# Kernel tuning notes

Measured on AMD Instinct MI355X. Metric: run time of the kernel, lower is better.

Reference implementation:

```python
import jax, jax.numpy as jnp
import numpy as np

H = 2048      # hidden_size
NH = 16       # num_heads
HD = H // NH  # head_dim
B, T = 2, 2048


def setup_inputs() -> dict:
    key = jax.random.key(0)
    ks = jax.random.split(key, 5)
    s = 1.0 / np.sqrt(H)
    return {
        "x": jax.random.normal(ks[0], (B, T, H), dtype=jnp.float32),
        "wq": jax.random.normal(ks[1], (H, H), dtype=jnp.float32) * s,
        "bq": jnp.zeros((H,), dtype=jnp.float32),
        "wk": jax.random.normal(ks[2], (H, H), dtype=jnp.float32) * s,
        "bk": jnp.zeros((H,), dtype=jnp.float32),
        "wv": jax.random.normal(ks[3], (H, H), dtype=jnp.float32) * s,
        "bv": jnp.zeros((H,), dtype=jnp.float32),
        "wo": jax.random.normal(ks[4], (H, H), dtype=jnp.float32) * s,
        "bo": jnp.zeros((H,), dtype=jnp.float32),
    }


def reference(x, wq, bq, wk, bk, wv, bv, wo, bo):
    Bx, Tx, C = x.shape
    # projections (torch Linear: x @ W.T + b)
    q = x @ wq.T + bq
    k = x @ wk.T + bk
    v = x @ wv.T + bv
    # [B, T, H] -> [B, NH, T, HD]
    q = q.reshape(Bx, Tx, NH, HD).transpose(0, 2, 1, 3)
    k = k.reshape(Bx, Tx, NH, HD).transpose(0, 2, 1, 3)
    v = v.reshape(Bx, Tx, NH, HD).transpose(0, 2, 1, 3)
    scale = 1.0 / np.sqrt(HD).astype(np.float32)
    scores = jnp.einsum('bhqd,bhkd->bhqk', q, k) * scale  # [B, NH, T, T]
    causal = jnp.tril(jnp.ones((Tx, Tx), dtype=bool))
    scores = jnp.where(causal[None, None], scores, -jnp.inf)
    attn = jax.nn.softmax(scores, axis=-1)
    out = jnp.einsum('bhqk,bhkd->bhqd', attn, v)  # [B, NH, T, HD]
    out = out.transpose(0, 2, 1, 3).reshape(Bx, Tx, C)
    return out @ wo.T + bo
```

## Files before the change

kernel.cpp:

```cpp
#include <hip/hip_runtime.h>
#include <stdint.h>

constexpr int H_  = 2048;
constexpr int NH_ = 16;
constexpr int HD_ = 128;
constexpr int B_  = 2;
constexpr int T_  = 2048;
constexpr int M_  = B_ * T_;

typedef unsigned short u16;
typedef __bf16 bf16x8 __attribute__((ext_vector_type(8)));
typedef float  f32x4  __attribute__((ext_vector_type(4)));

constexpr float C1_ = 0.08838834764831845f * 1.4426950408889634f;

template <int N> struct IC { static constexpr int value = N; };

__device__ __forceinline__ u16 f2bf(float f) {
  uint32_t u = __builtin_bit_cast(uint32_t, f);
  u += 0x7fffu + ((u >> 16) & 1u);
  return (u16)(u >> 16);
}

__device__ __forceinline__ uint32_t cvtpk(float lo, float hi) {
  uint32_t r;
  asm("v_cvt_pk_bf16_f32 %0, %1, %2" : "=v"(r) : "v"(lo), "v"(hi));
  return r;
}

__device__ __forceinline__ void gload_lds16(const void* g, void* lds) {
  auto gp = (const __attribute__((address_space(1))) uint32_t*)(uintptr_t)g;
  auto lp = (__attribute__((address_space(3))) uint32_t*)(uint32_t)(uintptr_t)lds;
  __builtin_amdgcn_global_load_lds(gp, lp, 16, 0, 0);
}

__device__ __forceinline__ f32x4 mfma16(bf16x8 a, bf16x8 b, f32x4 c) {
  return __builtin_amdgcn_mfma_f32_16x16x32_bf16(a, b, c, 0, 0, 0);
}

__global__ __launch_bounds__(512) void cvt5_kernel(
    const float4* __restrict__ x,  const float4* __restrict__ wq,
    const float4* __restrict__ wk, const float4* __restrict__ wv,
    const float4* __restrict__ wo, ushort4* __restrict__ dst) {
  const int bid = blockIdx.x, tid = threadIdx.x;
  const float4* src;
  size_t idx, dof;
  if (bid < 4096) {
    src = x; idx = (size_t)bid * 512 + tid; dof = 0;
  } else {
    int w = (bid - 4096) >> 11;
    int r = (bid - 4096) & 2047;
    idx = (size_t)r * 512 + tid;
    dof = 2097152u + (size_t)w * 1048576u;
    src = (w == 0) ? wq : (w == 1) ? wk : (w == 2) ? wv : wo;
  }
  float4 v = src[idx];
  ushort4 o;
  o.x = f2bf(v.x); o.y = f2bf(v.y); o.z = f2bf(v.z); o.w = f2bf(v.w);
  dst[dof + idx] = o;
}

__device__ __forceinline__ void gemm256_core(const u16* __restrict__ A,
                                             const u16* __restrict__ Bm,
                                             const float* __restrict__ bias,
                                             void* __restrict__ Cout,
                                             int bid, int outmode,
                                             float oscale) {
  __shared__ u16 As[3][256 * 64];
  __shared__ u16 Bs[3][128 * 64];
  constexpr int Kg = H_;
  constexpr int NT = Kg / 64;
  const int tid = threadIdx.x;
  const int wave = tid >> 6, lane = tid & 63, l15 = lane & 15, lhi = lane >> 4;
  const int tm = bid & 15, tn = bid >> 4;
  const int m0 = tm << 8, n0 = tn << 7;
  const int wr = wave >> 1, wc = wave & 1;

  f32x4 acc[4][4] = {};

  const u16* pA[4];
  const u16* pB[2];
  {
    int o = tid * 16;
    int row = o >> 7;
    int sw  = o ^ ((row & 7) << 4);
    int c8  = (sw >> 4) & 7;
#pragma unroll
    for (int a = 0; a < 4; ++a)
      pA[a] = A + (size_t)(m0 + a * 64 + row) * Kg + c8 * 8;
#pragma unroll
    for (int a = 0; a < 2; ++a)
      pB[a] = Bm + (size_t)(n0 + a * 64 + row) * Kg + c8 * 8;
  }
  const int ldsoff = wave * 1024;

  int obA[2][4], obB[2][4];
#pragma unroll
  for (int kk = 0; kk < 2; ++kk) {
#pragma unroll
    for (int mi = 0; mi < 4; ++mi) {
      int rowA = wr * 64 + mi * 16 + l15;
      obA[kk][mi] = (rowA * 128 + kk * 64 + lhi * 16) ^ ((rowA & 7) << 4);
      int rowB = wc * 64 + mi * 16 + l15;
      obB[kk][mi] = (rowB * 128 + kk * 64 + lhi * 16) ^ ((rowB & 7) << 4);
    }
  }

  auto stageA = [&](int kt, auto bufc, int a) {
    constexpr int BUF = decltype(bufc)::value;
    gload_lds16(pA[a] + kt * 64,
                (char*)&As[BUF][0] + a * 8192 + ldsoff);
  };
  auto stageB = [&](int kt, auto bufc, int a) {
    constexpr int BUF = decltype(bufc)::value;
    gload_lds16(pB[a] + kt * 64,
                (char*)&Bs[BUF][0] + a * 8192 + ldsoff);
  };

  stageB(0, IC<0>{}, 0); stageB(0, IC<0>{}, 1);
  stageA(0, IC<0>{}, 0); stageA(0, IC<0>{}, 1);
  stageA(0, IC<0>{}, 2); stageA(0, IC<0>{}, 3);
  stageB(1, IC<1>{}, 0); stageB(1, IC<1>{}, 1);
  stageA(1, IC<1>{}, 0); stageA(1, IC<1>{}, 1);
  stageA(1, IC<1>{}, 2); stageA(1, IC<1>{}, 3);
  asm volatile("s_waitcnt vmcnt(6)" ::: "memory");
  __builtin_amdgcn_s_barrier();
  asm volatile("" ::: "memory");

  auto tile = [&](int kt, auto bufc) {
    constexpr int BUF = decltype(bufc)::value;
    constexpr int NXT = (BUF + 2) % 3;
    const bool hn2 = (kt + 2 < NT);
    const char* Ab = (const char*)&As[BUF][0];
    const char* Bb = (const char*)&Bs[BUF][0];
    bf16x8 a0, a1, b0, b1, b2, b3;

    a0 = *(const bf16x8*)(Ab + obA[0][0]); a1 = *(const bf16x8*)(Ab + obA[0][1]);
    b0 = *(const bf16x8*)(Bb + obB[0][0]); b1 = *(const bf16x8*)(Bb + obB[0][1]);
    b2 = *(const bf16x8*)(Bb + obB[0][2]); b3 = *(const bf16x8*)(Bb + obB[0][3]);
    if (hn2) { stageB(kt + 2, IC<NXT>{}, 0); stageB(kt + 2, IC<NXT>{}, 1); }
    __builtin_amdgcn_s_barrier(); asm volatile("" ::: "memory");
    __builtin_amdgcn_s_setprio(1);
    acc[0][0] = mfma16(a0, b0, acc[0][0]); acc[0][1] = mfma16(a0, b1, acc[0][1]);
    acc[0][2] = mfma16(a0, b2, acc[0][2]); acc[0][3] = mfma16(a0, b3, acc[0][3]);
    acc[1][0] = mfma16(a1, b0, acc[1][0]); acc[1][1] = mfma16(a1, b1, acc[1][1]);
    acc[1][2] = mfma16(a1, b2, acc[1][2]); acc[1][3] = mfma16(a1, b3, acc[1][3]);
    __builtin_amdgcn_s_setprio(0);
    __builtin_amdgcn_s_barrier(); asm volatile("" ::: "memory");

    a0 = *(const bf16x8*)(Ab + obA[0][2]); a1 = *(const bf16x8*)(Ab + obA[0][3]);
    if (hn2) { stageA(kt + 2, IC<NXT>{}, 0); stageA(kt + 2, IC<NXT>{}, 1); }
    __builtin_amdgcn_s_barrier(); asm volatile("" ::: "memory");
    __builtin_amdgcn_s_setprio(1);
    acc[2][0] = mfma16(a0, b0, acc[2][0]); acc[2][1] = mfma16(a0, b1, acc[2][1]);
    acc[2][2] = mfma16(a0, b2, acc[2][2]); acc[2][3] = mfma16(a0, b3, acc[2][3]);
    acc[3][0] = mfma16(a1, b0, acc[3][0]); acc[3][1] = mfma16(a1, b1, acc[3][1]);
    acc[3][2] = mfma16(a1, b2, acc[3][2]); acc[3][3] = mfma16(a1, b3, acc[3][3]);
    __builtin_amdgcn_s_setprio(0);
    __builtin_amdgcn_s_barrier(); asm volatile("" ::: "memory");

    a0 = *(const bf16x8*)(Ab + obA[1][0]); a1 = *(const bf16x8*)(Ab + obA[1][1]);
    b0 = *(const bf16x8*)(Bb + obB[1][0]); b1 = *(const bf16x8*)(Bb + obB[1][1]);
    b2 = *(const bf16x8*)(Bb + obB[1][2]); b3 = *(const bf16x8*)(Bb + obB[1][3]);
    if (hn2) { stageA(kt + 2, IC<NXT>{}, 2); stageA(kt + 2, IC<NXT>{}, 3); }
    __builtin_amdgcn_s_barrier(); asm volatile("" ::: "memory");
    __builtin_amdgcn_s_setprio(1);
    acc[0][0] = mfma16(a0, b0, acc[0][0]); acc[0][1] = mfma16(a0, b1, acc[0][1]);
    acc[0][2] = mfma16(a0, b2, acc[0][2]); acc[0][3] = mfma16(a0, b3, acc[0][3]);
    acc[1][0] = mfma16(a1, b0, acc[1][0]); acc[1][1] = mfma16(a1, b1, acc[1][1]);
    acc[1][2] = mfma16(a1, b2, acc[1][2]); acc[1][3] = mfma16(a1, b3, acc[1][3]);
    __builtin_amdgcn_s_setprio(0);
    __builtin_amdgcn_s_barrier(); asm volatile("" ::: "memory");

    a0 = *(const bf16x8*)(Ab + obA[1][2]); a1 = *(const bf16x8*)(Ab + obA[1][3]);
    __builtin_amdgcn_s_barrier(); asm volatile("" ::: "memory");
    __builtin_amdgcn_s_setprio(1);
    acc[2][0] = mfma16(a0, b0, acc[2][0]); acc[2][1] = mfma16(a0, b1, acc[2][1]);
    acc[2][2] = mfma16(a0, b2, acc[2][2]); acc[2][3] = mfma16(a0, b3, acc[2][3]);
    acc[3][0] = mfma16(a1, b0, acc[3][0]); acc[3][1] = mfma16(a1, b1, acc[3][1]);
    acc[3][2] = mfma16(a1, b2, acc[3][2]); acc[3][3] = mfma16(a1, b3, acc[3][3]);
    __builtin_amdgcn_s_setprio(0);
    if (hn2)
      asm volatile("s_waitcnt vmcnt(6) lgkmcnt(0)" ::: "memory");
    else
      asm volatile("s_waitcnt vmcnt(0) lgkmcnt(0)" ::: "memory");
    __builtin_amdgcn_s_barrier(); asm volatile("" ::: "memory");
  };

#pragma unroll 1
  for (int kt = 0; kt < 30; kt += 3) {
    tile(kt,     IC<0>{});
    tile(kt + 1, IC<1>{});
    tile(kt + 2, IC<2>{});
  }
  tile(30, IC<0>{});
  tile(31, IC<1>{});

  float bv[4];
#pragma unroll
  for (int ni = 0; ni < 4; ++ni) bv[ni] = bias[n0 + wc * 64 + ni * 16 + l15];

  if (outmode == 2) {
    const int b = m0 >> 11;
    const int tbase = (m0 & 2047) + wr * 64 + lhi * 4;
#pragma unroll
    for (int mi = 0; mi < 4; ++mi) {
#pragma unroll
      for (int ni = 0; ni < 4; ++ni) {
        int n = n0 + wc * 64 + ni * 16 + l15;
        ushort4 pk;
        pk.x = f2bf(acc[mi][ni][0] + bv[ni]);
        pk.y = f2bf(acc[mi][ni][1] + bv[ni]);
        pk.z = f2bf(acc[mi][ni][2] + bv[ni]);
        pk.w = f2bf(acc[mi][ni][3] + bv[ni]);
        *(ushort4*)((u16*)Cout + (size_t)(b * 2048 + n) * T_ + tbase +
                    mi * 16) = pk;
      }
    }
  } else {
#pragma unroll
    for (int mi = 0; mi < 4; ++mi) {
#pragma unroll
      for (int ni = 0; ni < 4; ++ni) {
        int n = n0 + wc * 64 + ni * 16 + l15;
#pragma unroll
        for (int r = 0; r < 4; ++r) {
          int m = m0 + wr * 64 + mi * 16 + lhi * 4 + r;
          float v = (acc[mi][ni][r] + bv[ni]) * oscale;
          if (outmode == 1)
            ((float*)Cout)[(size_t)m * H_ + n] = v;
          else
            ((u16*)Cout)[(size_t)m * H_ + n] = f2bf(v);
        }
      }
    }
  }
}

template <int OUTMODE>
__global__ __launch_bounds__(512, 1) void gemm256_bt_k(
    const u16* __restrict__ A, const u16* __restrict__ Bm,
    const float* __restrict__ bias, void* __restrict__ Cout, float oscale) {
  gemm256_core(A, Bm, bias, Cout, blockIdx.x, OUTMODE, oscale);
}

__global__ __launch_bounds__(256, 2) void attn_kernel(
    const u16* __restrict__ Q, const u16* __restrict__ K,
    const u16* __restrict__ Vt, u16* __restrict__ ctx) {
  __shared__ u16 Ks[2][64 * 128];
  __shared__ u16 Vs[2][128 * 64];
  __shared__ u16 Ps[4][1024];

  const int tid = threadIdx.x, wave = tid >> 6, lane = tid & 63;
  const int l15 = lane & 15, lhi = lane >> 4;

  const int bid = blockIdx.x;
  const int xcd = bid & 7, idx = bid >> 3;
  const int bh = xcd * 4 + (idx & 3);
  const int qj = idx >> 2;
  const int qi = (qj < 8) ? qj : 23 - qj;
  const int b = bh >> 4, h = bh & 15;
  const int qb0 = qi, qb1 = 31 - qi;

  const float THR = 11.5f;
  const float NI  = -__builtin_inff();

  auto stage = [&](auto bufc, int kv0) {
    constexpr int BUF = decltype(bufc)::value;
#pragma unroll
    for (int is = 0; is < 4; ++is) {
      {
        int o_ = is * 4096 + tid * 16;
        int row = o_ >> 8;
        int sw = o_ ^ (((o_ >> 8) & 7) << 4);
        int c8 = (sw >> 4) & 15;
        gload_lds16(K + (size_t)(b * T_ + kv0 + row) * H_ + h * HD_ + c8 * 8,
                    &Ks[BUF][0] + (is * 2048 + wave * 512));
      }
      {
        int o_ = is * 4096 + tid * 16;
        int row = o_ >> 7;
        int sw = o_ ^ (((o_ >> 7) & 7) << 4);
        int t8 = (sw >> 4) & 7;
        gload_lds16(Vt + (size_t)(bh * HD_ + row) * T_ + kv0 + t8 * 8,
                    &Vs[BUF][0] + (is * 4096 / 2 + wave * 512));
      }
    }
  };

  bf16x8 qc0[4], qc1[4];
  {
    const u16* q0p =
        Q + (size_t)(b * T_ + qb0 * 64 + wave * 16 + l15) * H_ + h * HD_ + lhi * 8;
    const u16* q1p =
        Q + (size_t)(b * T_ + qb1 * 64 + wave * 16 + l15) * H_ + h * HD_ + lhi * 8;
#pragma unroll
    for (int kk = 0; kk < 4; ++kk) {
      qc0[kk] = *(const bf16x8*)(q0p + kk * 32);
      qc1[kk] = *(const bf16x8*)(q1p + kk * 32);
    }
  }

  f32x4 o0[8] = {}, o1[8] = {};
  float m20 = NI, lr0 = 0.f, m21 = NI, lr1 = 0.f;

  auto comp = [&](f32x4 (&o)[8], float& m2, float& lr, bf16x8 (&qf)[4],
                  int q0, bool diag, int kv0, auto bufc) {
    constexpr int BUF = decltype(bufc)::value;
    const int qrow = q0 + l15;

    f32x4 sv[4];
    __builtin_amdgcn_s_setprio(1);
#pragma unroll
    for (int kt = 0; kt < 4; ++kt) {
      f32x4 sacc = {0.f, 0.f, 0.f, 0.f};
#pragma unroll
      for (int kk = 0; kk < 4; ++kk) {
        int row = kt * 16 + l15;
        int ob = (row * 256 + kk * 64 + lhi * 16) ^ ((row & 7) << 4);
        bf16x8 kf = *(const bf16x8*)((const char*)&Ks[BUF][0] + ob);
        sacc = mfma16(kf, qf[kk], sacc);
      }
      sv[kt] = sacc;
    }
    __builtin_amdgcn_s_setprio(0);

    float pmax2;
    {
      float pm[4];
      if (diag) {
#pragma unroll
        for (int kt = 0; kt < 4; ++kt) {
          int key0 = kv0 + kt * 16 + lhi * 4;
#pragma unroll
          for (int r = 0; r < 4; ++r)
            sv[kt][r] = (key0 + r <= qrow) ? sv[kt][r] : NI;
          pm[kt] = fmaxf(fmaxf(sv[kt][0], sv[kt][1]),
                         fmaxf(sv[kt][2], sv[kt][3]));
        }
      } else {
#pragma unroll
        for (int kt = 0; kt < 4; ++kt)
          pm[kt] = fmaxf(fmaxf(sv[kt][0], sv[kt][1]),
                         fmaxf(sv[kt][2], sv[kt][3]));
      }
      pmax2 = fmaxf(fmaxf(pm[0], pm[1]), fmaxf(pm[2], pm[3]));
    }
    pmax2 = fmaxf(pmax2, __shfl_xor(pmax2, 16));
    pmax2 = fmaxf(pmax2, __shfl_xor(pmax2, 32));

    if (__any(pmax2 - m2 > THR)) {
      float mn = fmaxf(m2, pmax2);
      float al = exp2f(m2 - mn);
      m2 = mn;
      lr *= al;
      float alo[4];
#pragma unroll
      for (int r = 0; r < 4; ++r) alo[r] = __shfl(al, lhi * 4 + r);
#pragma unroll
      for (int dt = 0; dt < 8; ++dt)
#pragma unroll
        for (int r = 0; r < 4; ++r) o[dt][r] *= alo[r];
    }

    float rsk[4];
#pragma unroll
    for (int kt = 0; kt < 4; ++kt) {
#pragma unroll
      for (int r = 0; r < 4; ++r) sv[kt][r] = exp2f(sv[kt][r] - m2);
      rsk[kt] = (sv[kt][0] + sv[kt][1]) + (sv[kt][2] + sv[kt][3]);
    }
    float rs = (rsk[0] + rsk[1]) + (rsk[2] + rsk[3]);
    rs += __shfl_xor(rs, 16);
    rs += __shfl_xor(rs, 32);
    lr += rs;

#pragma unroll
    for (int kt = 0; kt < 4; ++kt) {
      int slot = kt * 2 + (lhi >> 1);
      uint2 pk;
      pk.x = cvtpk(sv[kt][0], sv[kt][1]);
      pk.y = cvtpk(sv[kt][2], sv[kt][3]);
      *(uint2*)&Ps[wave][slot * 128 + ((l15 * 8) ^ ((slot & 7) << 3)) +
                         (lhi & 1) * 4] = pk;
    }
    asm volatile("" ::: "memory");

    __builtin_amdgcn_s_setprio(1);
#pragma unroll
    for (int ks = 0; ks < 2; ++ks) {
      int slot = ks * 4 + lhi;
      bf16x8 pf = *(const bf16x8*)&Ps[wave][slot * 128 +
                                            ((l15 * 8) ^ ((slot & 7) << 3))];
#pragma unroll
      for (int dt = 0; dt < 8; ++dt) {
        int row = dt * 16 + l15;
        int ob = (row * 128 + ks * 64 + lhi * 16) ^ ((row & 7) << 4);
        bf16x8 vf = *(const bf16x8*)((const char*)&Vs[BUF][0] + ob);
        o[dt] = mfma16(pf, vf, o[dt]);
      }
    }
    __builtin_amdgcn_s_setprio(0);
    asm volatile("" ::: "memory");
  };

  auto flushout = [&](f32x4 (&o)[8], float lr, int qtile) {
    float invo[4];
    float inv = 1.0f / lr;
#pragma unroll
    for (int r = 0; r < 4; ++r) invo[r] = __shfl(inv, lhi * 4 + r);
    int q0 = qtile * 64 + wave * 16;
#pragma unroll
    for (int dt = 0; dt < 8; ++dt)
#pragma unroll
      for (int r = 0; r < 4; ++r)
        ctx[(size_t)(b * T_ + q0 + lhi * 4 + r) * H_ + h * HD_ + dt * 16 +
            l15] = f2bf(o[dt][r] * invo[r]);
  };

  stage(IC<0>{}, 0);
  asm volatile("s_waitcnt vmcnt(0)" ::: "memory");
  __builtin_amdgcn_s_barrier();
  asm volatile("" ::: "memory");

  auto body = [&](int t, auto bufc) {
    constexpr int BUF = decltype(bufc)::value;
    if (t < qb1) stage(IC<BUF ^ 1>{}, (t + 1) * 64);
    if (t < qb1)
      asm volatile("s_waitcnt vmcnt(8)" ::: "memory");
    else
      asm volatile("s_waitcnt vmcnt(0)" ::: "memory");
    __builtin_amdgcn_s_barrier();
    asm volatile("" ::: "memory");

    const int kv0 = t * 64;
    comp(o1, m21, lr1, qc1, qb1 * 64 + wave * 16, t == qb1, kv0, bufc);
    if (t <= qb0)
      comp(o0, m20, lr0, qc0, qb0 * 64 + wave * 16, t == qb0, kv0, bufc);

    asm volatile("s_waitcnt lgkmcnt(0)" ::: "memory");
    __builtin_amdgcn_s_barrier();
    asm volatile("" ::: "memory");
  };

#pragma unroll 1
  for (int t2 = 0; t2 + 1 <= qb1; t2 += 2) {
    body(t2, IC<0>{});
    body(t2 + 1, IC<1>{});
  }
  if ((qb1 & 1) == 0) body(qb1, IC<0>{});

  flushout(o0, lr0, qb0);
  flushout(o1, lr1, qb1);
}

extern "C" void kernel_launch(void* const* d_in, const int* in_sizes, int n_in,
                              void* d_out, int out_size, void* d_ws,
                              size_t ws_size, hipStream_t stream) {
  const float* x  = (const float*)d_in[0];
  const float* wq = (const float*)d_in[1];
  const float* bq = (const float*)d_in[2];
  const float* wk = (const float*)d_in[3];
  const float* bk = (const float*)d_in[4];
  const float* wv = (const float*)d_in[5];
  const float* bv = (const float*)d_in[6];
  const float* wo = (const float*)d_in[7];
  const float* bo = (const float*)d_in[8];

  char* ws = (char*)d_ws;
  constexpr size_t SZ_X = (size_t)M_ * H_ * 2;
  constexpr size_t SZ_W = (size_t)H_ * H_ * 2;
  u16* xb  = (u16*)(ws);
  u16* wqb = (u16*)(ws + SZ_X);
  u16* wkb = (u16*)(ws + SZ_X + 1 * SZ_W);
  u16* wvb = (u16*)(ws + SZ_X + 2 * SZ_W);
  u16* wob = (u16*)(ws + SZ_X + 3 * SZ_W);
  u16* Qb  = (u16*)(ws + 1 * SZ_X + 4 * SZ_W);
  u16* Kb  = (u16*)(ws + 2 * SZ_X + 4 * SZ_W);
  u16* Vtb = (u16*)(ws + 3 * SZ_X + 4 * SZ_W);
  u16* ctx = xb;

  cvt5_kernel<<<12288, 512, 0, stream>>>((const float4*)x, (const float4*)wq,
                                         (const float4*)wk, (const float4*)wv,
                                         (const float4*)wo, (ushort4*)ws);

  gemm256_bt_k<0><<<256, 512, 0, stream>>>(xb, wqb, bq, Qb, C1_);
  gemm256_bt_k<0><<<256, 512, 0, stream>>>(xb, wkb, bk, Kb, 1.0f);
  gemm256_bt_k<2><<<256, 512, 0, stream>>>(xb, wvb, bv, Vtb, 1.0f);

  attn_kernel<<<512, 256, 0, stream>>>(Qb, Kb, Vtb, ctx);

  gemm256_bt_k<1><<<256, 512, 0, stream>>>(ctx, wob, bo, d_out, 1.0f);
}
```

Before: 226.2 us.

## Switch projection GEMM from 16x16x32 to 32x32x16 MFMA tiles

```diff
diff --git a/kernel.cpp b/kernel.cpp
--- a/kernel.cpp
+++ b/kernel.cpp
@@ -11,6 +11,7 @@
 typedef unsigned short u16;
 typedef __bf16 bf16x8 __attribute__((ext_vector_type(8)));
 typedef float  f32x4  __attribute__((ext_vector_type(4)));
+typedef float  f32x16 __attribute__((ext_vector_type(16)));
 
 constexpr float C1_ = 0.08838834764831845f * 1.4426950408889634f;
 
@@ -36,6 +37,9 @@
 
 __device__ __forceinline__ f32x4 mfma16(bf16x8 a, bf16x8 b, f32x4 c) {
   return __builtin_amdgcn_mfma_f32_16x16x32_bf16(a, b, c, 0, 0, 0);
+}
+__device__ __forceinline__ f32x16 mfma32(bf16x8 a, bf16x8 b, f32x16 c) {
+  return __builtin_amdgcn_mfma_f32_32x32x16_bf16(a, b, c, 0, 0, 0);
 }
 
 __global__ __launch_bounds__(512) void cvt5_kernel(
@@ -71,12 +75,13 @@
   constexpr int Kg = H_;
   constexpr int NT = Kg / 64;
   const int tid = threadIdx.x;
-  const int wave = tid >> 6, lane = tid & 63, l15 = lane & 15, lhi = lane >> 4;
+  const int wave = tid >> 6, lane = tid & 63;
+  const int l31 = lane & 31, lhi5 = lane >> 5;
   const int tm = bid & 15, tn = bid >> 4;
   const int m0 = tm << 8, n0 = tn << 7;
   const int wr = wave >> 1, wc = wave & 1;
 
-  f32x4 acc[4][4] = {};
+  f32x16 acc[2][2] = {};
 
   const u16* pA[4];
   const u16* pB[2];
@@ -94,15 +99,15 @@
   }
   const int ldsoff = wave * 1024;
 
-  int obA[2][4], obB[2][4];
-#pragma unroll
-  for (int kk = 0; kk < 2; ++kk) {
-#pragma unroll
-    for (int mi = 0; mi < 4; ++mi) {
-      int rowA = wr * 64 + mi * 16 + l15;
-      obA[kk][mi] = (rowA * 128 + kk * 64 + lhi * 16) ^ ((rowA & 7) << 4);
-      int rowB = wc * 64 + mi * 16 + l15;
-      obB[kk][mi] = (rowB * 128 + kk * 64 + lhi * 16) ^ ((rowB & 7) << 4);
+  int obA[4][2], obB[4][2];
+#pragma unroll
+  for (int ks = 0; ks < 4; ++ks) {
+#pragma unroll
+    for (int i = 0; i < 2; ++i) {
+      int rowA = wr * 64 + i * 32 + l31;
+      obA[ks][i] = (rowA * 128 + ks * 32 + lhi5 * 16) ^ ((rowA & 7) << 4);
+      int rowB = wc * 64 + i * 32 + l31;
+      obB[ks][i] = (rowB * 128 + ks * 32 + lhi5 * 16) ^ ((rowB & 7) << 4);
     }
   }
 
@@ -133,52 +138,39 @@
     const bool hn2 = (kt + 2 < NT);
     const char* Ab = (const char*)&As[BUF][0];
     const char* Bb = (const char*)&Bs[BUF][0];
-    bf16x8 a0, a1, b0, b1, b2, b3;
-
-    a0 = *(const bf16x8*)(Ab + obA[0][0]); a1 = *(const bf16x8*)(Ab + obA[0][1]);
-    b0 = *(const bf16x8*)(Bb + obB[0][0]); b1 = *(const bf16x8*)(Bb + obB[0][1]);
-    b2 = *(const bf16x8*)(Bb + obB[0][2]); b3 = *(const bf16x8*)(Bb + obB[0][3]);
-    if (hn2) { stageB(kt + 2, IC<NXT>{}, 0); stageB(kt + 2, IC<NXT>{}, 1); }
+    bf16x8 a00, a01, a10, a11, b00, b01, b10, b11;
+
+    a00 = *(const bf16x8*)(Ab + obA[0][0]); a01 = *(const bf16x8*)(Ab + obA[0][1]);
+    b00 = *(const bf16x8*)(Bb + obB[0][0]); b01 = *(const bf16x8*)(Bb + obB[0][1]);
+    a10 = *(const bf16x8*)(Ab + obA[1][0]); a11 = *(const bf16x8*)(Ab + obA[1][1]);
+    b10 = *(const bf16x8*)(Bb + obB[1][0]); b11 = *(const bf16x8*)(Bb + obB[1][1]);
+    if (hn2) {
+      stageB(kt + 2, IC<NXT>{}, 0); stageB(kt + 2, IC<NXT>{}, 1);
+      stageA(kt + 2, IC<NXT>{}, 0);
+    }
     __builtin_amdgcn_s_barrier(); asm volatile("" ::: "memory");
     __builtin_amdgcn_s_setprio(1);
-    acc[0][0] = mfma16(a0, b0, acc[0][0]); acc[0][1] = mfma16(a0, b1, acc[0][1]);
-    acc[0][2] = mfma16(a0, b2, acc[0][2]); acc[0][3] = mfma16(a0, b3, acc[0][3]);
-    acc[1][0] = mfma16(a1, b0, acc[1][0]); acc[1][1] = mfma16(a1, b1, acc[1][1]);
-    acc[1][2] = mfma16(a1, b2, acc[1][2]); acc[1][3] = mfma16(a1, b3, acc[1][3]);
+    acc[0][0] = mfma32(a00, b00, acc[0][0]); acc[0][1] = mfma32(a00, b01, acc[0][1]);
+    acc[1][0] = mfma32(a01, b00, acc[1][0]); acc[1][1] = mfma32(a01, b01, acc[1][1]);
+    acc[0][0] = mfma32(a10, b10, acc[0][0]); acc[0][1] = mfma32(a10, b11, acc[0][1]);
+    acc[1][0] = mfma32(a11, b10, acc[1][0]); acc[1][1] = mfma32(a11, b11, acc[1][1]);
     __builtin_amdgcn_s_setprio(0);
     __builtin_amdgcn_s_barrier(); asm volatile("" ::: "memory");
 
-    a0 = *(const bf16x8*)(Ab + obA[0][2]); a1 = *(const bf16x8*)(Ab + obA[0][3]);
-    if (hn2) { stageA(kt + 2, IC<NXT>{}, 0); stageA(kt + 2, IC<NXT>{}, 1); }
+    a00 = *(const bf16x8*)(Ab + obA[2][0]); a01 = *(const bf16x8*)(Ab + obA[2][1]);
+    b00 = *(const bf16x8*)(Bb + obB[2][0]); b01 = *(const bf16x8*)(Bb + obB[2][1]);
+    a10 = *(const bf16x8*)(Ab + obA[3][0]); a11 = *(const bf16x8*)(Ab + obA[3][1]);
+    b10 = *(const bf16x8*)(Bb + obB[3][0]); b11 = *(const bf16x8*)(Bb + obB[3][1]);
+    if (hn2) {
+      stageA(kt + 2, IC<NXT>{}, 1); stageA(kt + 2, IC<NXT>{}, 2);
+      stageA(kt + 2, IC<NXT>{}, 3);
+    }
     __builtin_amdgcn_s_barrier(); asm volatile("" ::: "memory");
     __builtin_amdgcn_s_setprio(1);
-    acc[2][0] = mfma16(a0, b0, acc[2][0]); acc[2][1] = mfma16(a0, b1, acc[2][1]);
-    acc[2][2] = mfma16(a0, b2, acc[2][2]); acc[2][3] = mfma16(a0, b3, acc[2][3]);
-    acc[3][0] = mfma16(a1, b0, acc[3][0]); acc[3][1] = mfma16(a1, b1, acc[3][1]);
-    acc[3][2] = mfma16(a1, b2, acc[3][2]); acc[3][3] = mfma16(a1, b3, acc[3][3]);
-    __builtin_amdgcn_s_setprio(0);
-    __builtin_amdgcn_s_barrier(); asm volatile("" ::: "memory");
-
-    a0 = *(const bf16x8*)(Ab + obA[1][0]); a1 = *(const bf16x8*)(Ab + obA[1][1]);
-    b0 = *(const bf16x8*)(Bb + obB[1][0]); b1 = *(const bf16x8*)(Bb + obB[1][1]);
-    b2 = *(const bf16x8*)(Bb + obB[1][2]); b3 = *(const bf16x8*)(Bb + obB[1][3]);
-    if (hn2) { stageA(kt + 2, IC<NXT>{}, 2); stageA(kt + 2, IC<NXT>{}, 3); }
-    __builtin_amdgcn_s_barrier(); asm volatile("" ::: "memory");
-    __builtin_amdgcn_s_setprio(1);
-    acc[0][0] = mfma16(a0, b0, acc[0][0]); acc[0][1] = mfma16(a0, b1, acc[0][1]);
-    acc[0][2] = mfma16(a0, b2, acc[0][2]); acc[0][3] = mfma16(a0, b3, acc[0][3]);
-    acc[1][0] = mfma16(a1, b0, acc[1][0]); acc[1][1] = mfma16(a1, b1, acc[1][1]);
-    acc[1][2] = mfma16(a1, b2, acc[1][2]); acc[1][3] = mfma16(a1, b3, acc[1][3]);
-    __builtin_amdgcn_s_setprio(0);
-    __builtin_amdgcn_s_barrier(); asm volatile("" ::: "memory");
-
-    a0 = *(const bf16x8*)(Ab + obA[1][2]); a1 = *(const bf16x8*)(Ab + obA[1][3]);
-    __builtin_amdgcn_s_barrier(); asm volatile("" ::: "memory");
-    __builtin_amdgcn_s_setprio(1);
-    acc[2][0] = mfma16(a0, b0, acc[2][0]); acc[2][1] = mfma16(a0, b1, acc[2][1]);
-    acc[2][2] = mfma16(a0, b2, acc[2][2]); acc[2][3] = mfma16(a0, b3, acc[2][3]);
-    acc[3][0] = mfma16(a1, b0, acc[3][0]); acc[3][1] = mfma16(a1, b1, acc[3][1]);
-    acc[3][2] = mfma16(a1, b2, acc[3][2]); acc[3][3] = mfma16(a1, b3, acc[3][3]);
+    acc[0][0] = mfma32(a00, b00, acc[0][0]); acc[0][1] = mfma32(a00, b01, acc[0][1]);
+    acc[1][0] = mfma32(a01, b00, acc[1][0]); acc[1][1] = mfma32(a01, b01, acc[1][1]);
+    acc[0][0] = mfma32(a10, b10, acc[0][0]); acc[0][1] = mfma32(a10, b11, acc[0][1]);
+    acc[1][0] = mfma32(a11, b10, acc[1][0]); acc[1][1] = mfma32(a11, b11, acc[1][1]);
     __builtin_amdgcn_s_setprio(0);
     if (hn2)
       asm volatile("s_waitcnt vmcnt(6) lgkmcnt(0)" ::: "memory");
@@ -196,41 +188,46 @@
   tile(30, IC<0>{});
   tile(31, IC<1>{});
 
-  float bv[4];
-#pragma unroll
-  for (int ni = 0; ni < 4; ++ni) bv[ni] = bias[n0 + wc * 64 + ni * 16 + l15];
+  float bv[2];
+#pragma unroll
+  for (int ni = 0; ni < 2; ++ni) bv[ni] = bias[n0 + wc * 64 + ni * 32 + l31];
 
   if (outmode == 2) {
     const int b = m0 >> 11;
-    const int tbase = (m0 & 2047) + wr * 64 + lhi * 4;
-#pragma unroll
-    for (int mi = 0; mi < 4; ++mi) {
-#pragma unroll
-      for (int ni = 0; ni < 4; ++ni) {
-        int n = n0 + wc * 64 + ni * 16 + l15;
-        ushort4 pk;
-        pk.x = f2bf(acc[mi][ni][0] + bv[ni]);
-        pk.y = f2bf(acc[mi][ni][1] + bv[ni]);
-        pk.z = f2bf(acc[mi][ni][2] + bv[ni]);
-        pk.w = f2bf(acc[mi][ni][3] + bv[ni]);
-        *(ushort4*)((u16*)Cout + (size_t)(b * 2048 + n) * T_ + tbase +
-                    mi * 16) = pk;
+#pragma unroll
+    for (int mi = 0; mi < 2; ++mi) {
+#pragma unroll
+      for (int ni = 0; ni < 2; ++ni) {
+        int n = n0 + wc * 64 + ni * 32 + l31;
+#pragma unroll
+        for (int g = 0; g < 4; ++g) {
+          int t = (m0 & 2047) + wr * 64 + mi * 32 + g * 8 + lhi5 * 4;
+          ushort4 pk;
+          pk.x = f2bf(acc[mi][ni][g * 4 + 0] + bv[ni]);
+          pk.y = f2bf(acc[mi][ni][g * 4 + 1] + bv[ni]);
+          pk.z = f2bf(acc[mi][ni][g * 4 + 2] + bv[ni]);
+          pk.w = f2bf(acc[mi][ni][g * 4 + 3] + bv[ni]);
+          *(ushort4*)((u16*)Cout + (size_t)(b * 2048 + n) * T_ + t) = pk;
+        }
       }
     }
   } else {
 #pragma unroll
-    for (int mi = 0; mi < 4; ++mi) {
-#pragma unroll
-      for (int ni = 0; ni < 4; ++ni) {
-        int n = n0 + wc * 64 + ni * 16 + l15;
-#pragma unroll
-        for (int r = 0; r < 4; ++r) {
-          int m = m0 + wr * 64 + mi * 16 + lhi * 4 + r;
-          float v = (acc[mi][ni][r] + bv[ni]) * oscale;
-          if (outmode == 1)
-            ((float*)Cout)[(size_t)m * H_ + n] = v;
-          else
-            ((u16*)Cout)[(size_t)m * H_ + n] = f2bf(v);
+    for (int mi = 0; mi < 2; ++mi) {
+#pragma unroll
+      for (int ni = 0; ni < 2; ++ni) {
+        int n = n0 + wc * 64 + ni * 32 + l31;
+#pragma unroll
+        for (int g = 0; g < 4; ++g) {
+#pragma unroll
+          for (int j = 0; j < 4; ++j) {
+            int m = m0 + wr * 64 + mi * 32 + g * 8 + lhi5 * 4 + j;
+            float v = (acc[mi][ni][g * 4 + j] + bv[ni]) * oscale;
+            if (outmode == 1)
+              ((float*)Cout)[(size_t)m * H_ + n] = v;
+            else
+              ((u16*)Cout)[(size_t)m * H_ + n] = f2bf(v);
+          }
         }
       }
     }
```

Result: slower. 243.4 us (+7.6%).
